# Performance work log

Measured on AMD Instinct MI355X. Metric: run time of the kernel, lower is better.

## Reference

```python
import jax, jax.numpy as jnp
import numpy as np

DEPTH = 100000


def setup_inputs() -> dict:
    key = jax.random.key(0)
    k1, _ = jax.random.split(key)
    B, S = 1024, 200
    tokens = jax.random.randint(k1, (B, S), 0, DEPTH, dtype=jnp.int32)
    # tf.one_hot on_value=1.0 broadcast to every token position
    on_values = jnp.ones((B, S), dtype=jnp.float32)
    return {"tokens": tokens, "on_values": on_values}


def reference(tokens, on_values):
    """Equivalent to sum(one_hot(tokens, depth), axis=1) -> (B, depth) counts,
    computed via scatter-add without materializing the (B, S, depth) one-hot."""
    B, S = tokens.shape
    tokens = tokens.astype(jnp.int32)
    batch_idx = jnp.arange(B, dtype=jnp.int32)[:, None]  # (B, 1) broadcast over S
    counts = jnp.zeros((B, DEPTH), dtype=jnp.float32)
    counts = counts.at[batch_idx, tokens].add(on_values)
    return counts
```

## Files before the change

kernel.cpp:

```cpp
#include <hip/hip_runtime.h>


#define EMB_DEPTH 100000
#define EMB_SEQ   200

__global__ __launch_bounds__(256) void embedder_count_kernel(
    const int*   __restrict__ tokens,
    const float* __restrict__ on_values,
    float*       __restrict__ out)
{
    const int b   = blockIdx.x;
    const int tid = threadIdx.x;

    float* row = out + (size_t)b * EMB_DEPTH;
    float4* row4 = reinterpret_cast<float4*>(row);
    const float4 z = make_float4(0.0f, 0.0f, 0.0f, 0.0f);

    #pragma unroll 4
    for (int i = tid; i < EMB_DEPTH / 4; i += 256) {
        row4[i] = z;
    }

    __syncthreads();

    if (tid < EMB_SEQ) {
        const int   t = tokens[(size_t)b * EMB_SEQ + tid];
        const float v = on_values[(size_t)b * EMB_SEQ + tid];
        atomicAdd(row + t, v);
    }
}

extern "C" void kernel_launch(void* const* d_in, const int* in_sizes, int n_in,
                              void* d_out, int out_size, void* d_ws, size_t ws_size,
                              hipStream_t stream) {
    const int*   tokens    = (const int*)  d_in[0];
    const float* on_values = (const float*)d_in[1];
    float*       out       = (float*)      d_out;

    const int B = 1024;
    embedder_count_kernel<<<B, 256, 0, stream>>>(tokens, on_values, out);
}
```

Measured before the change: 96.44 us.

## Build per-segment counts in LDS and write each output row once

```diff
diff --git a/kernel.cpp b/kernel.cpp
--- a/kernel.cpp
+++ b/kernel.cpp
@@ -3,30 +3,38 @@
 
 #define EMB_DEPTH 100000
 #define EMB_SEQ   200
+#define NSEG      8
+#define SEGSZ     (EMB_DEPTH / NSEG)
 
-__global__ __launch_bounds__(256) void embedder_count_kernel(
+__global__ __launch_bounds__(256) void embedder_seg_kernel(
     const int*   __restrict__ tokens,
     const float* __restrict__ on_values,
     float*       __restrict__ out)
 {
-    const int b   = blockIdx.x;
+    __shared__ float cnt[SEGSZ];
+
     const int tid = threadIdx.x;
+    const int b   = blockIdx.x >> 3;
+    const int seg = blockIdx.x & (NSEG - 1);
+    const int lo  = seg * SEGSZ;
 
-    float* row = out + (size_t)b * EMB_DEPTH;
-    float4* row4 = reinterpret_cast<float4*>(row);
-    const float4 z = make_float4(0.0f, 0.0f, 0.0f, 0.0f);
-
-    #pragma unroll 4
-    for (int i = tid; i < EMB_DEPTH / 4; i += 256) {
-        row4[i] = z;
-    }
-
+    for (int i = tid; i < SEGSZ; i += 256) cnt[i] = 0.0f;
     __syncthreads();
 
     if (tid < EMB_SEQ) {
-        const int   t = tokens[(size_t)b * EMB_SEQ + tid];
-        const float v = on_values[(size_t)b * EMB_SEQ + tid];
-        atomicAdd(row + t, v);
+        const int t = tokens[(size_t)b * EMB_SEQ + tid];
+        const unsigned r = (unsigned)(t - lo);
+        if (r < (unsigned)SEGSZ) {
+            atomicAdd(&cnt[r], on_values[(size_t)b * EMB_SEQ + tid]);
+        }
+    }
+    __syncthreads();
+
+    float4* out4 = reinterpret_cast<float4*>(out + (size_t)b * EMB_DEPTH + lo);
+    const float4* c4 = reinterpret_cast<const float4*>(cnt);
+    #pragma unroll 4
+    for (int i = tid; i < SEGSZ / 4; i += 256) {
+        out4[i] = c4[i];
     }
 }
 
@@ -37,6 +45,6 @@
     const float* on_values = (const float*)d_in[1];
     float*       out       = (float*)      d_out;
 
-    const int B = 1024;
-    embedder_count_kernel<<<B, 256, 0, stream>>>(tokens, on_values, out);
+    const int B = in_sizes[0] / EMB_SEQ;
+    embedder_seg_kernel<<<B * NSEG, 256, 0, stream>>>(tokens, on_values, out);
 }
```

New measurement: 78.09 us. -19.0%, faster.

## Split row zero-fill and scatter-add into separate grid-stride kernels

Applied to the files above, without the earlier changes.

```diff
diff --git a/kernel.cpp b/kernel.cpp
--- a/kernel.cpp
+++ b/kernel.cpp
@@ -4,29 +4,26 @@
 #define EMB_DEPTH 100000
 #define EMB_SEQ   200
 
-__global__ __launch_bounds__(256) void embedder_count_kernel(
+__global__ __launch_bounds__(256) void zero_fill_kernel(
+    float4* __restrict__ out, int n4)
+{
+    const float4 z = make_float4(0.0f, 0.0f, 0.0f, 0.0f);
+    const int stride = gridDim.x * 256;
+    int i = blockIdx.x * 256 + threadIdx.x;
+    for (; i < n4; i += stride) out[i] = z;
+}
+
+__global__ __launch_bounds__(256) void scatter_add_kernel(
     const int*   __restrict__ tokens,
     const float* __restrict__ on_values,
-    float*       __restrict__ out)
+    float*       __restrict__ out,
+    int total)
 {
-    const int b   = blockIdx.x;
-    const int tid = threadIdx.x;
-
-    float* row = out + (size_t)b * EMB_DEPTH;
-    float4* row4 = reinterpret_cast<float4*>(row);
-    const float4 z = make_float4(0.0f, 0.0f, 0.0f, 0.0f);
-
-    #pragma unroll 4
-    for (int i = tid; i < EMB_DEPTH / 4; i += 256) {
-        row4[i] = z;
-    }
-
-    __syncthreads();
-
-    if (tid < EMB_SEQ) {
-        const int   t = tokens[(size_t)b * EMB_SEQ + tid];
-        const float v = on_values[(size_t)b * EMB_SEQ + tid];
-        atomicAdd(row + t, v);
+    const int i = blockIdx.x * 256 + threadIdx.x;
+    if (i < total) {
+        const int b = i / EMB_SEQ;
+        const int t = tokens[i];
+        atomicAdd(out + (size_t)b * EMB_DEPTH + t, on_values[i]);
     }
 }
 
@@ -37,6 +34,10 @@
     const float* on_values = (const float*)d_in[1];
     float*       out       = (float*)      d_out;
 
-    const int B = 1024;
-    embedder_count_kernel<<<B, 256, 0, stream>>>(tokens, on_values, out);
+    const int total = in_sizes[0];
+    const int n4    = out_size / 4;
+
+    zero_fill_kernel<<<2048, 256, 0, stream>>>((float4*)out, n4);
+    scatter_add_kernel<<<(total + 255) / 256, 256, 0, stream>>>(
+        tokens, on_values, out, total);
 }
```

Measured after the change: 118.8 us. 23.2% more time.
